# Kernel optimization log

Measured on AMD Instinct MI355X. Metric: run time of the kernel, lower is better.

The kernel has to match this reference:

```python
import jax, jax.numpy as jnp
import numpy as np

N = 50000          # num vertices
K = 16             # max padded neighbors
D = 256            # feature dim
H = 256            # num_hidddens


def setup_inputs() -> dict:
    key = jax.random.key(0)
    k1, k2, k3, k4, k5 = jax.random.split(key, 5)
    vertex_feat = jax.random.normal(k1, (N, D), dtype=jnp.float32)
    neighbors_idx = jax.random.randint(k2, (N, K), 0, N, dtype=jnp.int32)
    valid_lens = jax.random.randint(k3, (N,), 0, K + 1, dtype=jnp.int32)
    W = jax.random.normal(k4, (D, H), dtype=jnp.float32) * (1.0 / np.sqrt(D))
    B = jax.random.normal(k5, (D, H), dtype=jnp.float32) * (1.0 / np.sqrt(D))
    return {"vertex_feat": vertex_feat, "neighbors_idx": neighbors_idx,
            "valid_lens": valid_lens, "W": W, "B": B}


def reference(vertex_feat, neighbors_idx, valid_lens, W, B):
    # gather neighbor features: [N, K, D]
    nb = vertex_feat[neighbors_idx]
    # sequence mask over padded neighbor slots: [N, K]
    mask = (jnp.arange(K)[None, :] < valid_lens[:, None]).astype(vertex_feat.dtype)
    # masked sum then mean (valid_lens==0 -> divide by 1, matching tf.where guard)
    agg = jnp.einsum('nkd,nk->nd', nb, mask)
    denom = jnp.maximum(valid_lens, 1).astype(vertex_feat.dtype)
    agg = agg / denom[:, None]
    # dual dense (no bias) + relu
    out = jax.nn.relu(agg @ W + vertex_feat @ B)
    return out
```

## Files before the change

### kernel.cpp

```cpp
#include <hip/hip_runtime.h>
#include <stdint.h>


#define N_V   50000
#define KNB   16
#define D_F   256
#define H_F   256
#define K2    512
#define NPAD  50048

typedef __bf16 bf16x8 __attribute__((ext_vector_type(8)));
typedef float  f32x4  __attribute__((ext_vector_type(4)));
typedef unsigned short ushort8 __attribute__((ext_vector_type(8)));

static __device__ __forceinline__ unsigned short f2bf(float f) {
    union { float f; unsigned u; } v; v.f = f;
    unsigned u = v.u;
    u += 0x7fffu + ((u >> 16) & 1u);
    return (unsigned short)(u >> 16);
}
static __device__ __forceinline__ float bf2f(unsigned short u) {
    union { unsigned u; float f; } v; v.u = ((unsigned)u) << 16; return v.f;
}
static __device__ __forceinline__ void load16(const void* g, void* l) {
    __builtin_amdgcn_global_load_lds(
        (__attribute__((address_space(1))) void*)g,
        (__attribute__((address_space(3))) void*)l, 16, 0, 0);
}

__global__ __launch_bounds__(256) void vf_convert(
    const float* __restrict__ vf, unsigned short* __restrict__ vfb) {
    const int total = NPAD * (D_F / 8);
    for (int c = blockIdx.x * 256 + threadIdx.x; c < total; c += gridDim.x * 256) {
        int n = c >> 5;
        int off = (c & 31) * 8;
        ushort8 o;
        if (n < N_V) {
            const float4 a = *(const float4*)(vf + (size_t)n * D_F + off);
            const float4 b = *(const float4*)(vf + (size_t)n * D_F + off + 4);
            o[0]=f2bf(a.x); o[1]=f2bf(a.y); o[2]=f2bf(a.z); o[3]=f2bf(a.w);
            o[4]=f2bf(b.x); o[5]=f2bf(b.y); o[6]=f2bf(b.z); o[7]=f2bf(b.w);
        } else {
            o = (ushort8)(0);
        }
        *(ushort8*)(vfb + (size_t)n * D_F + off) = o;
    }
}

__global__ __launch_bounds__(256) void wbt_convert(
    const float* __restrict__ W, const float* __restrict__ Bm,
    unsigned short* __restrict__ WBt) {
    __shared__ unsigned short t[32][34];
    const int k0 = blockIdx.x * 32;
    const int h0 = blockIdx.y * 32;
    const int tid = threadIdx.x;
    {
        int r  = tid >> 3;
        int c4 = (tid & 7) * 4;
        int kg = k0 + r;
        const float* src = (kg < 256) ? (W  + (size_t)kg * H_F + h0 + c4)
                                      : (Bm + (size_t)(kg - 256) * H_F + h0 + c4);
        float4 v = *(const float4*)src;
        t[r][c4 + 0] = f2bf(v.x); t[r][c4 + 1] = f2bf(v.y);
        t[r][c4 + 2] = f2bf(v.z); t[r][c4 + 3] = f2bf(v.w);
    }
    __syncthreads();
    {
        int hh  = tid >> 3;
        int kk4 = (tid & 7) * 4;
        ushort4 o;
        o.x = t[kk4 + 0][hh]; o.y = t[kk4 + 1][hh];
        o.z = t[kk4 + 2][hh]; o.w = t[kk4 + 3][hh];
        *(ushort4*)(WBt + (size_t)(h0 + hh) * K2 + k0 + kk4) = o;
    }
}

__global__ __launch_bounds__(256) void gather_mean(
    const unsigned short* __restrict__ vfb, const int* __restrict__ nbr,
    const int* __restrict__ lens, unsigned short* __restrict__ aggb) {
    const int wave = threadIdx.x >> 6;
    const int lane = threadIdx.x & 63;
    const int n = blockIdx.x * 4 + wave;
    if (n >= NPAD) return;
    unsigned short* arow = aggb + (size_t)n * D_F;
    if (n >= N_V) {
        ushort4 z = {0, 0, 0, 0};
        *(ushort4*)(arow + lane * 4) = z;
        return;
    }
    const int len = lens[n];
    const int idx = nbr[(size_t)n * KNB + (lane & 15)];
    f32x4 acc = {0.f, 0.f, 0.f, 0.f};
#define ROW_(j) (*(const ushort4*)(vfb + (size_t)(j) * D_F + lane * 4))
#define ACC_(v) { acc[0] += bf2f(v.x); acc[1] += bf2f(v.y); \
                  acc[2] += bf2f(v.z); acc[3] += bf2f(v.w); }
    int k = 0;
    for (; k + 4 <= len; k += 4) {
        int j0 = __shfl(idx, k),     j1 = __shfl(idx, k + 1);
        int j2 = __shfl(idx, k + 2), j3 = __shfl(idx, k + 3);
        ushort4 v0 = ROW_(j0), v1 = ROW_(j1), v2 = ROW_(j2), v3 = ROW_(j3);
        ACC_(v0); ACC_(v1); ACC_(v2); ACC_(v3);
    }
    for (; k < len; ++k) {
        int j = __shfl(idx, k);
        ushort4 v = ROW_(j);
        ACC_(v);
    }
#undef ROW_
#undef ACC_
    const float inv = 1.0f / (float)(len > 0 ? len : 1);
    ushort4 o;
    o.x = f2bf(acc[0] * inv); o.y = f2bf(acc[1] * inv);
    o.z = f2bf(acc[2] * inv); o.w = f2bf(acc[3] * inv);
    *(ushort4*)(arow + lane * 4) = o;
}

__global__ __launch_bounds__(512) void gemm_relu(
    const unsigned short* __restrict__ aggb,
    const unsigned short* __restrict__ vfb,
    const unsigned short* __restrict__ WBt,
    float* __restrict__ out) {
    __shared__ char Alds[2][8192];
    __shared__ char Blds[2][16384];
    const int bm = blockIdx.x * 128;
    const int tid  = threadIdx.x;
    const int wave = tid >> 6, lane = tid & 63;
    const int wm = wave >> 2, wn = wave & 3;

    f32x4 acc[4][4];
    const f32x4 fzero = {0.f, 0.f, 0.f, 0.f};
#pragma unroll
    for (int i = 0; i < 4; ++i)
#pragma unroll
        for (int j = 0; j < 4; ++j) acc[i][j] = fzero;

    auto stage = [&](int buf, int t) {
        const int k0 = t * 32;
        {
            unsigned P = tid * 16u;
            unsigned L = P ^ (((P >> 6) & 3u) << 4);
            unsigned row = L >> 6, colb = L & 63u;
            const char* src = (k0 < 256)
                ? (const char*)aggb + (size_t)(bm + row) * 512 + k0 * 2 + colb
                : (const char*)vfb  + (size_t)(bm + row) * 512 + (k0 - 256) * 2 + colb;
            load16(src, Alds[buf] + wave * 1024);
        }
#pragma unroll
        for (int i = 0; i < 2; ++i) {
            unsigned P = i * 8192u + tid * 16u;
            unsigned L = P ^ (((P >> 6) & 3u) << 4);
            unsigned row = L >> 6, colb = L & 63u;
            const char* src = (const char*)WBt + (size_t)row * 1024 + k0 * 2 + colb;
            load16(src, Blds[buf] + i * 8192 + wave * 1024);
        }
    };

    stage(0, 0);
    __syncthreads();
    int cur = 0;
    for (int t = 0; t < 16; ++t) {
        if (t < 15) stage(cur ^ 1, t + 1);
        bf16x8 af[4], bfr[4];
#pragma unroll
        for (int mf = 0; mf < 4; ++mf) {
            unsigned r = wm * 64 + mf * 16 + (lane & 15);
            unsigned L = r * 64 + ((lane >> 4) << 4);
            unsigned P = L ^ (((L >> 6) & 3u) << 4);
            af[mf] = *(const bf16x8*)(Alds[cur] + P);
        }
#pragma unroll
        for (int nf = 0; nf < 4; ++nf) {
            unsigned r = wn * 64 + nf * 16 + (lane & 15);
            unsigned L = r * 64 + ((lane >> 4) << 4);
            unsigned P = L ^ (((L >> 6) & 3u) << 4);
            bfr[nf] = *(const bf16x8*)(Blds[cur] + P);
        }
#pragma unroll
        for (int mf = 0; mf < 4; ++mf)
#pragma unroll
            for (int nf = 0; nf < 4; ++nf)
                acc[mf][nf] = __builtin_amdgcn_mfma_f32_16x16x32_bf16(
                    af[mf], bfr[nf], acc[mf][nf], 0, 0, 0);
        __syncthreads();
        cur ^= 1;
    }

#pragma unroll
    for (int mf = 0; mf < 4; ++mf) {
        int row0 = bm + wm * 64 + mf * 16 + ((lane >> 4) << 2);
#pragma unroll
        for (int nf = 0; nf < 4; ++nf) {
            int col = wn * 64 + nf * 16 + (lane & 15);
            f32x4 v = acc[mf][nf];
#pragma unroll
            for (int i = 0; i < 4; ++i) {
                int row = row0 + i;
                if (row < N_V)
                    out[(size_t)row * H_F + col] = fmaxf(v[i], 0.0f);
            }
        }
    }
}

extern "C" void kernel_launch(void* const* d_in, const int* in_sizes, int n_in,
                              void* d_out, int out_size, void* d_ws, size_t ws_size,
                              hipStream_t stream) {
    const float* vf   = (const float*)d_in[0];
    const int*   nbr  = (const int*)d_in[1];
    const int*   lens = (const int*)d_in[2];
    const float* W    = (const float*)d_in[3];
    const float* Bm   = (const float*)d_in[4];
    float* out = (float*)d_out;

    unsigned short* aggb = (unsigned short*)d_ws;
    unsigned short* vfb  = aggb + (size_t)NPAD * D_F;
    unsigned short* WBt  = vfb + (size_t)NPAD * D_F;

    hipLaunchKernelGGL(vf_convert, dim3(2048), dim3(256), 0, stream, vf, vfb);
    hipLaunchKernelGGL(wbt_convert, dim3(16, 8), dim3(256), 0, stream, W, Bm, WBt);
    hipLaunchKernelGGL(gather_mean, dim3(NPAD / 4), dim3(256), 0, stream,
                       vfb, nbr, lens, aggb);
    hipLaunchKernelGGL(gemm_relu, dim3(NPAD / 128), dim3(512), 0, stream,
                       aggb, vfb, WBt, out);
}
```

Baseline: 167.3 us.

## Reorder to transform-then-aggregate: GEMM with concatenated [W|B] then gather projected rows

Uses linearity of the mean to compute Y = X·[W|B] once per vertex, then gathers neighbor rows of the XW half and adds the XB half before ReLU. The separate fp32-to-bf16 conversion pass is removed because the GEMM reads fp32 inputs and converts them in registers while staging into LDS. The aggregated-feature intermediate and the K=512 GEMM are replaced by a K=256, N=512 GEMM plus a gather-epilogue kernel. In exchange, the neighbor-summed values are bf16-rounded projections rather than bf16 features, which changes rounding behavior.

```diff
diff --git a/kernel.cpp b/kernel.cpp
--- a/kernel.cpp
+++ b/kernel.cpp
@@ -6,12 +6,11 @@
 #define KNB   16
 #define D_F   256
 #define H_F   256
-#define K2    512
+#define HK2   512
 #define NPAD  50048
 
 typedef __bf16 bf16x8 __attribute__((ext_vector_type(8)));
 typedef float  f32x4  __attribute__((ext_vector_type(4)));
-typedef unsigned short ushort8 __attribute__((ext_vector_type(8)));
 
 static __device__ __forceinline__ unsigned short f2bf(float f) {
     union { float f; unsigned u; } v; v.f = f;
@@ -28,38 +27,19 @@
         (__attribute__((address_space(3))) void*)l, 16, 0, 0);
 }
 
-__global__ __launch_bounds__(256) void vf_convert(
-    const float* __restrict__ vf, unsigned short* __restrict__ vfb) {
-    const int total = NPAD * (D_F / 8);
-    for (int c = blockIdx.x * 256 + threadIdx.x; c < total; c += gridDim.x * 256) {
-        int n = c >> 5;
-        int off = (c & 31) * 8;
-        ushort8 o;
-        if (n < N_V) {
-            const float4 a = *(const float4*)(vf + (size_t)n * D_F + off);
-            const float4 b = *(const float4*)(vf + (size_t)n * D_F + off + 4);
-            o[0]=f2bf(a.x); o[1]=f2bf(a.y); o[2]=f2bf(a.z); o[3]=f2bf(a.w);
-            o[4]=f2bf(b.x); o[5]=f2bf(b.y); o[6]=f2bf(b.z); o[7]=f2bf(b.w);
-        } else {
-            o = (ushort8)(0);
-        }
-        *(ushort8*)(vfb + (size_t)n * D_F + off) = o;
-    }
-}
-
 __global__ __launch_bounds__(256) void wbt_convert(
     const float* __restrict__ W, const float* __restrict__ Bm,
     unsigned short* __restrict__ WBt) {
-    __shared__ unsigned short t[32][34];
+    __shared__ unsigned short t[32][33];
     const int k0 = blockIdx.x * 32;
     const int h0 = blockIdx.y * 32;
     const int tid = threadIdx.x;
     {
         int r  = tid >> 3;
         int c4 = (tid & 7) * 4;
-        int kg = k0 + r;
-        const float* src = (kg < 256) ? (W  + (size_t)kg * H_F + h0 + c4)
-                                      : (Bm + (size_t)(kg - 256) * H_F + h0 + c4);
+        const float* src = (h0 < 256)
+            ? (W  + (size_t)(k0 + r) * H_F + h0 + c4)
+            : (Bm + (size_t)(k0 + r) * H_F + (h0 - 256) + c4);
         float4 v = *(const float4*)src;
         t[r][c4 + 0] = f2bf(v.x); t[r][c4 + 1] = f2bf(v.y);
         t[r][c4 + 2] = f2bf(v.z); t[r][c4 + 3] = f2bf(v.w);
@@ -71,27 +51,110 @@
         ushort4 o;
         o.x = t[kk4 + 0][hh]; o.y = t[kk4 + 1][hh];
         o.z = t[kk4 + 2][hh]; o.w = t[kk4 + 3][hh];
-        *(ushort4*)(WBt + (size_t)(h0 + hh) * K2 + k0 + kk4) = o;
-    }
-}
-
-__global__ __launch_bounds__(256) void gather_mean(
-    const unsigned short* __restrict__ vfb, const int* __restrict__ nbr,
-    const int* __restrict__ lens, unsigned short* __restrict__ aggb) {
+        *(ushort4*)(WBt + (size_t)(h0 + hh) * D_F + k0 + kk4) = o;
+    }
+}
+
+__global__ __launch_bounds__(512, 4) void gemm_y(
+    const float* __restrict__ vf,
+    const unsigned short* __restrict__ WBt,
+    unsigned short* __restrict__ Y) {
+    __shared__ char Alds[2][4096];
+    __shared__ char Blds[2][32768];
+    const int bm   = blockIdx.x * 64;
+    const int tid  = threadIdx.x;
+    const int wave = tid >> 6, lane = tid & 63;
+    const int wm   = wave >> 2, wn = wave & 3;
+
+    f32x4 acc[2][8];
+    const f32x4 fzero = {0.f, 0.f, 0.f, 0.f};
+#pragma unroll
+    for (int i = 0; i < 2; ++i)
+#pragma unroll
+        for (int j = 0; j < 8; ++j) acc[i][j] = fzero;
+
+    const int ar = tid >> 3;
+    const int ak = (tid & 7) * 4;
+    const int arow_g = (bm + ar < N_V) ? bm + ar : N_V - 1;
+    const float* aptr = vf + (size_t)arow_g * D_F + ak;
+    const unsigned aP = ar * 64u + (((unsigned)ak * 2u) ^ (((unsigned)ar & 3u) << 4));
+
+    unsigned boff[4];
+#pragma unroll
+    for (int i = 0; i < 4; ++i) {
+        unsigned P = i * 8192u + tid * 16u;
+        unsigned L = P ^ (((P >> 6) & 3u) << 4);
+        boff[i] = (L >> 6) * 512u + (L & 63u);
+    }
+
+    float4 aReg;
+    auto stageA_load = [&](int t) { aReg = *(const float4*)(aptr + t * 32); };
+    auto stageA_write = [&](int buf) {
+        ushort4 o;
+        o.x = f2bf(aReg.x); o.y = f2bf(aReg.y);
+        o.z = f2bf(aReg.z); o.w = f2bf(aReg.w);
+        *(ushort4*)(Alds[buf] + aP) = o;
+    };
+    auto stageB = [&](int buf, int t) {
+#pragma unroll
+        for (int i = 0; i < 4; ++i)
+            load16((const char*)WBt + boff[i] + t * 64,
+                   Blds[buf] + i * 8192 + wave * 1024);
+    };
+
+    stageA_load(0); stageB(0, 0); stageA_write(0);
+    __syncthreads();
+    int cur = 0;
+    for (int t = 0; t < 8; ++t) {
+        if (t < 7) { stageA_load(t + 1); stageB(cur ^ 1, t + 1); }
+        bf16x8 af[2];
+#pragma unroll
+        for (int mf = 0; mf < 2; ++mf) {
+            unsigned r = wm * 32u + mf * 16u + (lane & 15);
+            unsigned c = ((unsigned)lane >> 4) << 4;
+            af[mf] = *(const bf16x8*)(Alds[cur] + r * 64 + (c ^ ((r & 3u) << 4)));
+        }
+#pragma unroll
+        for (int nf = 0; nf < 8; ++nf) {
+            unsigned r = wn * 128u + nf * 16u + (lane & 15);
+            unsigned c = ((unsigned)lane >> 4) << 4;
+            bf16x8 bfr = *(const bf16x8*)(Blds[cur] + r * 64 + (c ^ ((r & 3u) << 4)));
+            acc[0][nf] = __builtin_amdgcn_mfma_f32_16x16x32_bf16(
+                af[0], bfr, acc[0][nf], 0, 0, 0);
+            acc[1][nf] = __builtin_amdgcn_mfma_f32_16x16x32_bf16(
+                af[1], bfr, acc[1][nf], 0, 0, 0);
+        }
+        if (t < 7) stageA_write(cur ^ 1);
+        __syncthreads();
+        cur ^= 1;
+    }
+
+#pragma unroll
+    for (int mf = 0; mf < 2; ++mf) {
+        int row0 = bm + wm * 32 + mf * 16 + ((lane >> 4) << 2);
+#pragma unroll
+        for (int nf = 0; nf < 8; ++nf) {
+            int col = wn * 128 + nf * 16 + (lane & 15);
+            f32x4 v = acc[mf][nf];
+#pragma unroll
+            for (int i = 0; i < 4; ++i)
+                Y[(size_t)(row0 + i) * HK2 + col] = f2bf(v[i]);
+        }
+    }
+}
+
+__global__ __launch_bounds__(256) void gather_out(
+    const unsigned short* __restrict__ Y, const int* __restrict__ nbr,
+    const int* __restrict__ lens, float* __restrict__ out) {
     const int wave = threadIdx.x >> 6;
     const int lane = threadIdx.x & 63;
     const int n = blockIdx.x * 4 + wave;
-    if (n >= NPAD) return;
-    unsigned short* arow = aggb + (size_t)n * D_F;
-    if (n >= N_V) {
-        ushort4 z = {0, 0, 0, 0};
-        *(ushort4*)(arow + lane * 4) = z;
-        return;
-    }
+    if (n >= N_V) return;
     const int len = lens[n];
     const int idx = nbr[(size_t)n * KNB + (lane & 15)];
+    const ushort4 y2 = *(const ushort4*)(Y + (size_t)n * HK2 + 256 + lane * 4);
     f32x4 acc = {0.f, 0.f, 0.f, 0.f};
-#define ROW_(j) (*(const ushort4*)(vfb + (size_t)(j) * D_F + lane * 4))
+#define ROW_(j) (*(const ushort4*)(Y + (size_t)(j) * HK2 + lane * 4))
 #define ACC_(v) { acc[0] += bf2f(v.x); acc[1] += bf2f(v.y); \
                   acc[2] += bf2f(v.z); acc[3] += bf2f(v.w); }
     int k = 0;
@@ -109,97 +172,12 @@
 #undef ROW_
 #undef ACC_
     const float inv = 1.0f / (float)(len > 0 ? len : 1);
-    ushort4 o;
-    o.x = f2bf(acc[0] * inv); o.y = f2bf(acc[1] * inv);
-    o.z = f2bf(acc[2] * inv); o.w = f2bf(acc[3] * inv);
-    *(ushort4*)(arow + lane * 4) = o;
-}
-
-__global__ __launch_bounds__(512) void gemm_relu(
-    const unsigned short* __restrict__ aggb,
-    const unsigned short* __restrict__ vfb,
-    const unsigned short* __restrict__ WBt,
-    float* __restrict__ out) {
-    __shared__ char Alds[2][8192];
-    __shared__ char Blds[2][16384];
-    const int bm = blockIdx.x * 128;
-    const int tid  = threadIdx.x;
-    const int wave = tid >> 6, lane = tid & 63;
-    const int wm = wave >> 2, wn = wave & 3;
-
-    f32x4 acc[4][4];
-    const f32x4 fzero = {0.f, 0.f, 0.f, 0.f};
-#pragma unroll
-    for (int i = 0; i < 4; ++i)
-#pragma unroll
-        for (int j = 0; j < 4; ++j) acc[i][j] = fzero;
-
-    auto stage = [&](int buf, int t) {
-        const int k0 = t * 32;
-        {
-            unsigned P = tid * 16u;
-            unsigned L = P ^ (((P >> 6) & 3u) << 4);
-            unsigned row = L >> 6, colb = L & 63u;
-            const char* src = (k0 < 256)
-                ? (const char*)aggb + (size_t)(bm + row) * 512 + k0 * 2 + colb
-                : (const char*)vfb  + (size_t)(bm + row) * 512 + (k0 - 256) * 2 + colb;
-            load16(src, Alds[buf] + wave * 1024);
-        }
-#pragma unroll
-        for (int i = 0; i < 2; ++i) {
-            unsigned P = i * 8192u + tid * 16u;
-            unsigned L = P ^ (((P >> 6) & 3u) << 4);
-            unsigned row = L >> 6, colb = L & 63u;
-            const char* src = (const char*)WBt + (size_t)row * 1024 + k0 * 2 + colb;
-            load16(src, Blds[buf] + i * 8192 + wave * 1024);
-        }
-    };
-
-    stage(0, 0);
-    __syncthreads();
-    int cur = 0;
-    for (int t = 0; t < 16; ++t) {
-        if (t < 15) stage(cur ^ 1, t + 1);
-        bf16x8 af[4], bfr[4];
-#pragma unroll
-        for (int mf = 0; mf < 4; ++mf) {
-            unsigned r = wm * 64 + mf * 16 + (lane & 15);
-            unsigned L = r * 64 + ((lane >> 4) << 4);
-            unsigned P = L ^ (((L >> 6) & 3u) << 4);
-            af[mf] = *(const bf16x8*)(Alds[cur] + P);
-        }
-#pragma unroll
-        for (int nf = 0; nf < 4; ++nf) {
-            unsigned r = wn * 64 + nf * 16 + (lane & 15);
-            unsigned L = r * 64 + ((lane >> 4) << 4);
-            unsigned P = L ^ (((L >> 6) & 3u) << 4);
-            bfr[nf] = *(const bf16x8*)(Blds[cur] + P);
-        }
-#pragma unroll
-        for (int mf = 0; mf < 4; ++mf)
-#pragma unroll
-            for (int nf = 0; nf < 4; ++nf)
-                acc[mf][nf] = __builtin_amdgcn_mfma_f32_16x16x32_bf16(
-                    af[mf], bfr[nf], acc[mf][nf], 0, 0, 0);
-        __syncthreads();
-        cur ^= 1;
-    }
-
-#pragma unroll
-    for (int mf = 0; mf < 4; ++mf) {
-        int row0 = bm + wm * 64 + mf * 16 + ((lane >> 4) << 2);
-#pragma unroll
-        for (int nf = 0; nf < 4; ++nf) {
-            int col = wn * 64 + nf * 16 + (lane & 15);
-            f32x4 v = acc[mf][nf];
-#pragma unroll
-            for (int i = 0; i < 4; ++i) {
-                int row = row0 + i;
-                if (row < N_V)
-                    out[(size_t)row * H_F + col] = fmaxf(v[i], 0.0f);
-            }
-        }
-    }
+    float4 o;
+    o.x = fmaxf(fmaf(acc[0], inv, bf2f(y2.x)), 0.f);
+    o.y = fmaxf(fmaf(acc[1], inv, bf2f(y2.y)), 0.f);
+    o.z = fmaxf(fmaf(acc[2], inv, bf2f(y2.z)), 0.f);
+    o.w = fmaxf(fmaf(acc[3], inv, bf2f(y2.w)), 0.f);
+    *(float4*)(out + (size_t)n * H_F + lane * 4) = o;
 }
 
 extern "C" void kernel_launch(void* const* d_in, const int* in_sizes, int n_in,
@@ -212,14 +190,11 @@
     const float* Bm   = (const float*)d_in[4];
     float* out = (float*)d_out;
 
-    unsigned short* aggb = (unsigned short*)d_ws;
-    unsigned short* vfb  = aggb + (size_t)NPAD * D_F;
-    unsigned short* WBt  = vfb + (size_t)NPAD * D_F;
-
-    hipLaunchKernelGGL(vf_convert, dim3(2048), dim3(256), 0, stream, vf, vfb);
-    hipLaunchKernelGGL(wbt_convert, dim3(16, 8), dim3(256), 0, stream, W, Bm, WBt);
-    hipLaunchKernelGGL(gather_mean, dim3(NPAD / 4), dim3(256), 0, stream,
-                       vfb, nbr, lens, aggb);
-    hipLaunchKernelGGL(gemm_relu, dim3(NPAD / 128), dim3(512), 0, stream,
-                       aggb, vfb, WBt, out);
-}
+    unsigned short* Y   = (unsigned short*)d_ws;
+    unsigned short* WBt = Y + (size_t)NPAD * HK2;
+
+    hipLaunchKernelGGL(wbt_convert, dim3(8, 16), dim3(256), 0, stream, W, Bm, WBt);
+    hipLaunchKernelGGL(gemm_y, dim3(NPAD / 64), dim3(512), 0, stream, vf, WBt, Y);
+    hipLaunchKernelGGL(gather_out, dim3(N_V / 4), dim3(256), 0, stream,
+                       Y, nbr, lens, out);
+}
```

Measured after the change: 168.8 us. About the same (+0.9%).
